# Optimization experiments

Measured on AMD Instinct MI355X. Metric: run time of the kernel, lower is better.

## Reference

```python
import jax, jax.numpy as jnp
import numpy as np
from math import factorial

ZS = np.array([0, 1])
NZ = 2
N_BASIS = 3
N_CHAN = N_BASIS * N_BASIS
N_RBF = 8
MAX_L = 3
CUTOFF = 5.5
P_CUT = 6
N_NODES = 10000
N_EDGES = 100000


def _lxlylz_list(max_l):
    out = []
    for l in range(max_l + 1):
        for lx in range(l, -1, -1):
            for ly in range(l - lx, -1, -1):
                out.append((lx, ly, l - lx - ly))
    return out

LXLYLZ = np.array(_lxlylz_list(MAX_L), dtype=np.int32)  # [n_ang, 3]; (0,0,0) is index 0
N_ANG = LXLYLZ.shape[0]  # 20 for max_l=3

# nu=2 rotational invariants: for each l>0, monomial indices with lx+ly+lz==l and multinomial prefactors
NU2 = []
for l in range(1, MAX_L + 1):
    idx = [i for i in range(N_ANG) if int(LXLYLZ[i].sum()) == l]
    pref = np.array([factorial(l) / (factorial(int(LXLYLZ[i][0])) * factorial(int(LXLYLZ[i][1])) * factorial(int(LXLYLZ[i][2]))) for i in idx], dtype=np.float32)
    NU2.append((np.array(idx, dtype=np.int32), pref))


def setup_inputs() -> dict:
    key = jax.random.key(0)
    ks = jax.random.split(key, 6)
    positions = jax.random.normal(ks[0], (N_NODES, 3), jnp.float32)
    atomic_numbers = jax.random.randint(ks[1], (N_NODES,), 0, NZ)
    edge_index = jax.random.randint(ks[2], (2, N_EDGES), 0, N_NODES)
    edge_lengths = jax.random.uniform(ks[3], (N_EDGES,), jnp.float32, 0.5, CUTOFF)
    edge_vectors = jax.random.normal(ks[4], (N_EDGES, 3), jnp.float32)
    W_embed = jax.random.normal(ks[5], (NZ, N_BASIS), jnp.float32) / np.sqrt(NZ)
    return dict(positions=positions, atomic_numbers=atomic_numbers, edge_index=edge_index,
                edge_lengths=edge_lengths, edge_vectors=edge_vectors, W_embed=W_embed)


def reference(positions, atomic_numbers, edge_index, edge_lengths, edge_vectors, W_embed):
    n_nodes = positions.shape[0]
    # node one-hot over zs -> linear embedding
    one_hot = (atomic_numbers[:, None] == jnp.asarray(ZS)[None, :]).astype(W_embed.dtype)
    emb = one_hot @ W_embed  # [N, n_basis]
    # directed edge-type encoding: outer product of sender/receiver embeddings
    enc = (emb[edge_index[0]][:, :, None] * emb[edge_index[1]][:, None, :]).reshape(-1, N_CHAN)  # [E, c]
    # Bessel radial basis * polynomial cutoff
    r = edge_lengths
    n = jnp.arange(1, N_RBF + 1, dtype=r.dtype)
    radial = jnp.sqrt(2.0 / CUTOFF) * jnp.sin(n[None, :] * jnp.pi * r[:, None] / CUTOFF) / r[:, None]
    u = r / CUTOFF
    p = P_CUT
    fc = (1.0 - 0.5 * (p + 1) * (p + 2) * u ** p + p * (p + 2) * u ** (p + 1)
          - 0.5 * p * (p + 1) * u ** (p + 2)) * (u < 1.0)
    radial = radial * fc[:, None]  # [E, n_rbf]
    # angular monomials x^lx y^ly z^lz of unit edge vectors
    unit = edge_vectors / jnp.linalg.norm(edge_vectors, axis=-1, keepdims=True)
    ang = jnp.prod(unit[:, None, :] ** jnp.asarray(LXLYLZ)[None, :, :], axis=-1)  # [E, n_ang]
    # fused 3-tensor edge product then scatter-sum to receiver nodes
    edge_attr = jnp.einsum('er,ea,ec->erac', radial, ang, enc)  # [E, n_rbf, n_ang, c]
    A = jax.ops.segment_sum(edge_attr, edge_index[1], num_segments=n_nodes)  # node_feat_A
    # symmetrize to invariants: nu=1 (l=0 monomial) + nu=2 per-l invariants
    feats = [A[:, :, 0:1, :]]
    for idx, pref in NU2:
        sel = A[:, :, jnp.asarray(idx), :]
        feats.append(jnp.sum(jnp.asarray(pref)[None, None, :, None] * sel * sel, axis=2, keepdims=True))
    B = jnp.concatenate(feats, axis=2)  # node_feat_B: [N, n_rbf, 1+max_l, c]
    return B
```

## Files before the change

kernel.cpp:

```cpp
#include <hip/hip_runtime.h>


#define NN    10000
#define NE    100000
#define NRBF  8
#define NANG  20
#define NCHAN 9
#define CAP   64
#define BROW  44
#define INV_CUT  (1.0f/5.5f)
#define PI_F     3.14159265358979323846f
#define RAD_NORM 0.6030226891555273f

__launch_bounds__(256, 4)
__global__ void scatter_k(const int* __restrict__ an, const int* __restrict__ ei,
                          int* __restrict__ cnt, int* __restrict__ lst) {
    int e = blockIdx.x * blockDim.x + threadIdx.x;
    if (e >= NE) return;
    int src = ei[e];
    int dst = ei[NE + e];
    int zs  = an[src];
    int pos = atomicAdd(&cnt[dst], 1);
    if (pos < CAP) lst[dst * CAP + pos] = e | (zs << 20);
}

__launch_bounds__(64, 4)
__global__ void node_k(const int* __restrict__ an, const float* __restrict__ elen,
                       const float* __restrict__ evec, const float* __restrict__ W,
                       const int* __restrict__ cnt, const int* __restrict__ lst,
                       float* __restrict__ out)
{
    __shared__ float sB[CAP * BROW];
    float* sA = sB;

    const int n   = blockIdx.x;
    const int tid = threadIdx.x;

    int deg = cnt[n]; if (deg > CAP) deg = CAP;
    const int zd = an[n];

    const float W0=W[0], W1=W[1], W2=W[2], W3=W[3], W4=W[4], W5=W[5];
    const float wd0 = zd ? W3 : W0, wd1 = zd ? W4 : W1, wd2 = zd ? W5 : W2;

    if (tid < deg) {
        const int v   = lst[n * CAP + tid];
        const int eid = v & 0xFFFFF;
        const int zs  = v >> 20;

        const float r  = elen[eid];
        const float vx = evec[3*eid+0], vy = evec[3*eid+1], vz = evec[3*eid+2];
        const float inv = rsqrtf(vx*vx + vy*vy + vz*vz);
        const float x = vx*inv, y = vy*inv, z = vz*inv;

        const float u  = r * INV_CUT;
        const float u2 = u*u, u6 = u2*u2*u2;
        const float fc = (u < 1.0f) ? (1.0f - 28.0f*u6 + 48.0f*u6*u - 21.0f*u6*u2)
                                    : 0.0f;
        const float scale = RAD_NORM * fc / r;
        float s1, c1;
        sincosf(PI_F * u, &s1, &c1);
        const float twoc = 2.0f * c1;
        float sp = 0.0f, s = s1;
        float rad[8];
        #pragma unroll
        for (int k = 0; k < 8; ++k) {
            rad[k] = scale * s;
            const float sn = twoc * s - sp;
            sp = s; s = sn;
        }

        const float xx = x*x, xy = x*y, xz = x*z, yy = y*y, yz = y*z, zz = z*z;
        const float ws0 = zs ? W3 : W0, ws1 = zs ? W4 : W1, ws2 = zs ? W5 : W2;

        float* B = &sB[tid * BROW];
        *(float4*)&B[0]  = make_float4(rad[0], rad[1], rad[2], rad[3]);
        *(float4*)&B[4]  = make_float4(rad[4], rad[5], rad[6], rad[7]);
        *(float4*)&B[8]  = make_float4(1.0f, x, y, z);
        *(float4*)&B[12] = make_float4(xx, xy, xz, yy);
        *(float4*)&B[16] = make_float4(yz, zz, x*xx, y*xx);
        *(float4*)&B[20] = make_float4(z*xx, x*yy, x*yz, x*zz);
        *(float4*)&B[24] = make_float4(y*yy, z*yy, y*zz, z*zz);
        *(float4*)&B[28] = make_float4(ws0*wd0, ws0*wd1, ws0*wd2, ws1*wd0);
        *(float4*)&B[32] = make_float4(ws1*wd1, ws1*wd2, ws2*wd0, ws2*wd1);
        B[36] = ws2*wd2;
    }
    __syncthreads();

    const int a0 = tid / 9,          c0 = tid - 9*a0;
    const int p1 = tid + 64,  a1 = p1 / 9, c1 = p1 - 9*a1;
    const int p2 = tid + 128, a2 = (tid < 52) ? p2 / 9 : 0,
                              c2 = (tid < 52) ? p2 - 9*(p2/9) : 0;
    float acc0[8] = {0,0,0,0,0,0,0,0};
    float acc1[8] = {0,0,0,0,0,0,0,0};
    float acc2[8] = {0,0,0,0,0,0,0,0};

    for (int e = 0; e < deg; ++e) {
        const float* B = &sB[e * BROW];
        const float4 r0 = *(const float4*)&B[0];
        const float4 r1 = *(const float4*)&B[4];
        const float pe0 = B[8 + a0] * B[28 + c0];
        const float pe1 = B[8 + a1] * B[28 + c1];
        const float pe2 = B[8 + a2] * B[28 + c2];
        acc0[0]=fmaf(r0.x,pe0,acc0[0]); acc0[1]=fmaf(r0.y,pe0,acc0[1]);
        acc0[2]=fmaf(r0.z,pe0,acc0[2]); acc0[3]=fmaf(r0.w,pe0,acc0[3]);
        acc0[4]=fmaf(r1.x,pe0,acc0[4]); acc0[5]=fmaf(r1.y,pe0,acc0[5]);
        acc0[6]=fmaf(r1.z,pe0,acc0[6]); acc0[7]=fmaf(r1.w,pe0,acc0[7]);
        acc1[0]=fmaf(r0.x,pe1,acc1[0]); acc1[1]=fmaf(r0.y,pe1,acc1[1]);
        acc1[2]=fmaf(r0.z,pe1,acc1[2]); acc1[3]=fmaf(r0.w,pe1,acc1[3]);
        acc1[4]=fmaf(r1.x,pe1,acc1[4]); acc1[5]=fmaf(r1.y,pe1,acc1[5]);
        acc1[6]=fmaf(r1.z,pe1,acc1[6]); acc1[7]=fmaf(r1.w,pe1,acc1[7]);
        acc2[0]=fmaf(r0.x,pe2,acc2[0]); acc2[1]=fmaf(r0.y,pe2,acc2[1]);
        acc2[2]=fmaf(r0.z,pe2,acc2[2]); acc2[3]=fmaf(r0.w,pe2,acc2[3]);
        acc2[4]=fmaf(r1.x,pe2,acc2[4]); acc2[5]=fmaf(r1.y,pe2,acc2[5]);
        acc2[6]=fmaf(r1.z,pe2,acc2[6]); acc2[7]=fmaf(r1.w,pe2,acc2[7]);
    }
    __syncthreads();

    #pragma unroll
    for (int r = 0; r < NRBF; ++r) {
        sA[r*180 + tid] = acc0[r];
        sA[r*180 + p1]  = acc1[r];
        if (tid < 52) sA[r*180 + p2] = acc2[r];
    }
    __syncthreads();

    for (int o = tid; o < NRBF*4*NCHAN; o += 64) {
        const int r = o / 36, rem = o - r*36, l = rem / 9, c = rem - (rem/9)*9;
        const float* Ar = &sA[r * 180 + c];
        float val;
        if (l == 0) {
            val = Ar[0];
        } else if (l == 1) {
            const float v1 = Ar[9], v2 = Ar[18], v3 = Ar[27];
            val = v1*v1 + v2*v2 + v3*v3;
        } else if (l == 2) {
            const float v0=Ar[36], v1=Ar[45], v2=Ar[54],
                        v3=Ar[63], v4=Ar[72], v5=Ar[81];
            val = v0*v0 + 2.0f*(v1*v1 + v2*v2 + v4*v4) + v3*v3 + v5*v5;
        } else {
            const float w0=Ar[90],  w1=Ar[99],  w2=Ar[108], w3=Ar[117], w4=Ar[126];
            const float w5=Ar[135], w6=Ar[144], w7=Ar[153], w8=Ar[162], w9=Ar[171];
            val = w0*w0 + w6*w6 + w9*w9
                + 3.0f*(w1*w1 + w2*w2 + w3*w3 + w5*w5 + w7*w7 + w8*w8)
                + 6.0f*w4*w4;
        }
        out[n * (NRBF*4*NCHAN) + o] = val;
    }
}

extern "C" void kernel_launch(void* const* d_in, const int* in_sizes, int n_in,
                              void* d_out, int out_size, void* d_ws, size_t ws_size,
                              hipStream_t stream) {
    const int*   an   = (const int*)d_in[1];
    const int*   ei   = (const int*)d_in[2];
    const float* elen = (const float*)d_in[3];
    const float* evec = (const float*)d_in[4];
    const float* W    = (const float*)d_in[5];
    float* out = (float*)d_out;

    int* cnt = (int*)d_ws;
    int* lst = cnt + NN;

    hipMemsetAsync(cnt, 0, NN * sizeof(int), stream);
    scatter_k<<<(NE + 255)/256, 256, 0, stream>>>(an, ei, cnt, lst);
    node_k<<<NN, 64, 0, stream>>>(an, elen, evec, W, cnt, lst, out);
}
```

Measured before the change: 95.33 us.

## Factor channel encoding out of edge loop via species-split accumulation

The 9-channel encoding is a product of sender and receiver embeddings. The receiver part is constant per node and the sender part depends only on a binary species. So the edge loop now accumulates radial×angular sums split by sender species, using a ballot mask, and applies the weights once at the end. This cuts per-edge FMAs from roughly 24 per thread to at most 6, and shrinks the shared-memory row. The cost is a small epilogue and reliance on there being exactly two species.

```diff
diff --git a/kernel.cpp b/kernel.cpp
--- a/kernel.cpp
+++ b/kernel.cpp
@@ -7,7 +7,7 @@
 #define NANG  20
 #define NCHAN 9
 #define CAP   64
-#define BROW  44
+#define BROW  28
 #define INV_CUT  (1.0f/5.5f)
 #define PI_F     3.14159265358979323846f
 #define RAD_NORM 0.6030226891555273f
@@ -38,14 +38,13 @@
 
     int deg = cnt[n]; if (deg > CAP) deg = CAP;
     const int zd = an[n];
+    const float W0=W[0], W1=W[1], W2=W[2], W3=W[3], W4=W[4], W5=W[5];
 
-    const float W0=W[0], W1=W[1], W2=W[2], W3=W[3], W4=W[4], W5=W[5];
-    const float wd0 = zd ? W3 : W0, wd1 = zd ? W4 : W1, wd2 = zd ? W5 : W2;
-
+    int zsv = 0;
     if (tid < deg) {
         const int v   = lst[n * CAP + tid];
         const int eid = v & 0xFFFFF;
-        const int zs  = v >> 20;
+        zsv = v >> 20;
 
         const float r  = elen[eid];
         const float vx = evec[3*eid+0], vy = evec[3*eid+1], vz = evec[3*eid+2];
@@ -70,8 +69,6 @@
         }
 
         const float xx = x*x, xy = x*y, xz = x*z, yy = y*y, yz = y*z, zz = z*z;
-        const float ws0 = zs ? W3 : W0, ws1 = zs ? W4 : W1, ws2 = zs ? W5 : W2;
-
         float* B = &sB[tid * BROW];
         *(float4*)&B[0]  = make_float4(rad[0], rad[1], rad[2], rad[3]);
         *(float4*)&B[4]  = make_float4(rad[4], rad[5], rad[6], rad[7]);
@@ -80,47 +77,52 @@
         *(float4*)&B[16] = make_float4(yz, zz, x*xx, y*xx);
         *(float4*)&B[20] = make_float4(z*xx, x*yy, x*yz, x*zz);
         *(float4*)&B[24] = make_float4(y*yy, z*yy, y*zz, z*zz);
-        *(float4*)&B[28] = make_float4(ws0*wd0, ws0*wd1, ws0*wd2, ws1*wd0);
-        *(float4*)&B[32] = make_float4(ws1*wd1, ws1*wd2, ws2*wd0, ws2*wd1);
-        B[36] = ws2*wd2;
+    }
+    const unsigned long long zmask = __ballot(zsv != 0);
+    __syncthreads();
+
+    const int r0 = tid & 7;
+    const int a0 = tid >> 3;
+    float s00=0.f, s01=0.f, s02=0.f;
+    float s10=0.f, s11=0.f, s12=0.f;
+
+    for (int e = 0; e < deg; ++e) {
+        const float* B = &sB[e * BROW];
+        const float z1 = (float)((zmask >> e) & 1ULL);
+        const float z0 = 1.0f - z1;
+        const float rd = B[r0];
+        const float v0 = rd * B[8 + a0];
+        const float v1 = rd * B[16 + a0];
+        s00 = fmaf(v0, z0, s00); s10 = fmaf(v0, z1, s10);
+        s01 = fmaf(v1, z0, s01); s11 = fmaf(v1, z1, s11);
+        if (tid < 32) {
+            const float v2 = rd * B[24 + a0];
+            s02 = fmaf(v2, z0, s02); s12 = fmaf(v2, z1, s12);
+        }
     }
     __syncthreads();
 
-    const int a0 = tid / 9,          c0 = tid - 9*a0;
-    const int p1 = tid + 64,  a1 = p1 / 9, c1 = p1 - 9*a1;
-    const int p2 = tid + 128, a2 = (tid < 52) ? p2 / 9 : 0,
-                              c2 = (tid < 52) ? p2 - 9*(p2/9) : 0;
-    float acc0[8] = {0,0,0,0,0,0,0,0};
-    float acc1[8] = {0,0,0,0,0,0,0,0};
-    float acc2[8] = {0,0,0,0,0,0,0,0};
-
-    for (int e = 0; e < deg; ++e) {
-        const float* B = &sB[e * BROW];
-        const float4 r0 = *(const float4*)&B[0];
-        const float4 r1 = *(const float4*)&B[4];
-        const float pe0 = B[8 + a0] * B[28 + c0];
-        const float pe1 = B[8 + a1] * B[28 + c1];
-        const float pe2 = B[8 + a2] * B[28 + c2];
-        acc0[0]=fmaf(r0.x,pe0,acc0[0]); acc0[1]=fmaf(r0.y,pe0,acc0[1]);
-        acc0[2]=fmaf(r0.z,pe0,acc0[2]); acc0[3]=fmaf(r0.w,pe0,acc0[3]);
-        acc0[4]=fmaf(r1.x,pe0,acc0[4]); acc0[5]=fmaf(r1.y,pe0,acc0[5]);
-        acc0[6]=fmaf(r1.z,pe0,acc0[6]); acc0[7]=fmaf(r1.w,pe0,acc0[7]);
-        acc1[0]=fmaf(r0.x,pe1,acc1[0]); acc1[1]=fmaf(r0.y,pe1,acc1[1]);
-        acc1[2]=fmaf(r0.z,pe1,acc1[2]); acc1[3]=fmaf(r0.w,pe1,acc1[3]);
-        acc1[4]=fmaf(r1.x,pe1,acc1[4]); acc1[5]=fmaf(r1.y,pe1,acc1[5]);
-        acc1[6]=fmaf(r1.z,pe1,acc1[6]); acc1[7]=fmaf(r1.w,pe1,acc1[7]);
-        acc2[0]=fmaf(r0.x,pe2,acc2[0]); acc2[1]=fmaf(r0.y,pe2,acc2[1]);
-        acc2[2]=fmaf(r0.z,pe2,acc2[2]); acc2[3]=fmaf(r0.w,pe2,acc2[3]);
-        acc2[4]=fmaf(r1.x,pe2,acc2[4]); acc2[5]=fmaf(r1.y,pe2,acc2[5]);
-        acc2[6]=fmaf(r1.z,pe2,acc2[6]); acc2[7]=fmaf(r1.w,pe2,acc2[7]);
+    const float wd0 = zd ? W3 : W0, wd1 = zd ? W4 : W1, wd2 = zd ? W5 : W2;
+    {
+        const float t00 = W0*s00 + W3*s10, t01 = W1*s00 + W4*s10, t02 = W2*s00 + W5*s10;
+        float* Ap = &sA[r0*180 + a0*9];
+        Ap[0]=t00*wd0; Ap[1]=t00*wd1; Ap[2]=t00*wd2;
+        Ap[3]=t01*wd0; Ap[4]=t01*wd1; Ap[5]=t01*wd2;
+        Ap[6]=t02*wd0; Ap[7]=t02*wd1; Ap[8]=t02*wd2;
     }
-    __syncthreads();
-
-    #pragma unroll
-    for (int r = 0; r < NRBF; ++r) {
-        sA[r*180 + tid] = acc0[r];
-        sA[r*180 + p1]  = acc1[r];
-        if (tid < 52) sA[r*180 + p2] = acc2[r];
+    {
+        const float t10 = W0*s01 + W3*s11, t11 = W1*s01 + W4*s11, t12 = W2*s01 + W5*s11;
+        float* Ap = &sA[r0*180 + (8 + a0)*9];
+        Ap[0]=t10*wd0; Ap[1]=t10*wd1; Ap[2]=t10*wd2;
+        Ap[3]=t11*wd0; Ap[4]=t11*wd1; Ap[5]=t11*wd2;
+        Ap[6]=t12*wd0; Ap[7]=t12*wd1; Ap[8]=t12*wd2;
+    }
+    if (tid < 32) {
+        const float t20 = W0*s02 + W3*s12, t21 = W1*s02 + W4*s12, t22 = W2*s02 + W5*s12;
+        float* Ap = &sA[r0*180 + (16 + a0)*9];
+        Ap[0]=t20*wd0; Ap[1]=t20*wd1; Ap[2]=t20*wd2;
+        Ap[3]=t21*wd0; Ap[4]=t21*wd1; Ap[5]=t21*wd2;
+        Ap[6]=t22*wd0; Ap[7]=t22*wd1; Ap[8]=t22*wd2;
     }
     __syncthreads();
 
```

Result: faster. 90.38 us (-5.2%).
